# Kernel optimization log

Measured on AMD Instinct MI355X. Metric: run time of the kernel, lower is better.

Reference implementation:

```python
import jax, jax.numpy as jnp
import numpy as np

B, N, H, IN, OUT, AXES = 128, 32, 128, 1, 10, 4


def setup_inputs() -> dict:
    key = jax.random.key(0)
    ks = jax.random.split(key, 6)
    s = 0.05
    return {
        "x": jax.random.normal(ks[0], (B, N, N), jnp.float32),
        "Wx": jax.random.normal(ks[1], (AXES, IN, 3 * H), jnp.float32) * s,
        "U1": jax.random.normal(ks[2], (AXES, H, 3 * H), jnp.float32) * s,
        "U2": jax.random.normal(ks[3], (AXES, H, 3 * H), jnp.float32) * s,
        "b": jnp.zeros((AXES, 3 * H), jnp.float32),
        "Wo": jax.random.normal(ks[4], (AXES * H, OUT), jnp.float32) * s,
        "bo": jnp.zeros((OUT,), jnp.float32),
    }


def _mdgru_cell(xj, h_top, h_left, Wx, U1, U2, b):
    # xj: (B, IN); h_top/h_left: (B, H). Two-predecessor GRU cell.
    gx = xj @ Wx + b          # (B, 3H)
    g1 = h_top @ U1           # (B, 3H)
    g2 = h_left @ U2          # (B, 3H)
    xr, xz, xn = jnp.split(gx, 3, axis=-1)
    r1, z1, n1 = jnp.split(g1, 3, axis=-1)
    r2, z2, n2 = jnp.split(g2, 3, axis=-1)
    r = jax.nn.sigmoid(xr + r1 + r2)
    z = jax.nn.sigmoid(xz + z1 + z2)
    n = jnp.tanh(xn + r * (n1 + n2))
    return (1.0 - z) * n + z * 0.5 * (h_top + h_left)


def _scan_dir(img, Wx, U1, U2, b):
    # img: (N_rows, N_cols, B), oriented so scan runs top-left -> bottom-right.
    n_cols, bsz = img.shape[1], img.shape[2]
    h0 = jnp.zeros((bsz, H), img.dtype)

    def row_step(last_row, x_row):  # last_row: (N_cols, B, H); x_row: (N_cols, B)
        def col_step(h_left, inp):
            xj, h_top = inp
            h = _mdgru_cell(xj[:, None], h_top, h_left, Wx, U1, U2, b)
            return h, h
        _, row = jax.lax.scan(col_step, h0, (x_row, last_row))
        return row, row[-1]

    _, finals = jax.lax.scan(row_step, jnp.zeros((n_cols, bsz, H), img.dtype), img)
    return finals[-1]  # (B, H): hidden at the terminal corner


def reference(x, Wx, U1, U2, b, Wo, bo):
    # x: (B, N, N). Four diagonal scan directions via flips.
    flips = [(False, False), (True, False), (False, True), (True, True)]
    hs = []
    for a, (fi, fj) in enumerate(flips):
        xd = x
        if fi:
            xd = jnp.flip(xd, axis=1)
        if fj:
            xd = jnp.flip(xd, axis=2)
        img = jnp.transpose(xd, (1, 2, 0))  # (N_rows, N_cols, B)
        hs.append(_scan_dir(img, Wx[a], U1[a], U2[a], b[a]))
    final_hidden = jnp.concatenate(hs, axis=1)  # (B, 4H)
    return jax.nn.log_softmax(final_hidden @ Wo + bo, axis=1)
```

## Files before the change

kernel.cpp:

```cpp
#include <hip/hip_runtime.h>
#include <type_traits>


#define B_ 128
#define N_ 32
#define H_ 128
#define TH 384
#define KK 256

#define PLSTR 2640
#define BUFSTR 10560
#define PSTRIDE 21120
#define XDSTR 8064

typedef short bf16x8 __attribute__((ext_vector_type(8)));
typedef float f32x4 __attribute__((ext_vector_type(4)));

__device__ inline ushort f2bf(float f) {
    return (ushort)((__float_as_uint(f) + 0x8000u) >> 16);
}
__device__ inline ushort f2bf_rne(float f) {
    unsigned u = __float_as_uint(f);
    return (ushort)((u + 0x7FFFu + ((u >> 16) & 1u)) >> 16);
}

#define NL2E -1.44269504088896f

__global__ void conv_u(const float* __restrict__ U1, const float* __restrict__ U2,
                       ushort* __restrict__ ubf) {
    __shared__ float t[32][33];
    int bx = blockIdx.x;
    int amat = bx / 48, tile = bx % 48;
    int kt = tile / 12, ntl = tile % 12;
    int a = amat >> 1, mat = amat & 1;
    int kk0 = kt * 32, n0 = ntl * 32;
    int tx = threadIdx.x, ty = threadIdx.y;
    const float* U = mat ? U2 : U1;
#pragma unroll
    for (int r = 0; r < 4; r++)
        t[ty + r * 8][tx] = U[(a * H_ + kk0 + ty + r * 8) * TH + n0 + tx];
    __syncthreads();
#pragma unroll
    for (int r = 0; r < 4; r++) {
        int n = n0 + ty + r * 8;
        int kkl = kk0 + tx;
        ubf[(a * TH + n) * KK + mat * H_ + kkl] = f2bf_rne(t[tx][ty + r * 8]);
    }
}

__global__ __launch_bounds__(512, 2) void scan_all(
    const float* __restrict__ x, const float* __restrict__ Wx,
    const float* __restrict__ bvec, const ushort* __restrict__ ubf,
    float* __restrict__ finals) {

    __shared__ __align__(16) char hbf_c[2 * PSTRIDE];
    __shared__ __align__(16) char xd_c[2 * XDSTR];

    int bx = blockIdx.x;
    int a = bx >> 6, chunk = bx & 63;
    int tid = threadIdx.x;
    int lane = tid & 63, wn = tid >> 6;
    int l16 = lane & 15, lg = lane >> 4;

    for (int idx = tid; idx < (2 * PSTRIDE) / 4; idx += 512) ((unsigned*)hbf_c)[idx] = 0u;
    for (int idx = tid; idx < (2 * XDSTR) / 4; idx += 512) ((unsigned*)xd_c)[idx] = 0u;
    __syncthreads();

    const float* xg = x + (chunk * 2) * (N_ * N_);
    for (int cell = tid; cell < 2048; cell += 512) {
        int P = cell >> 10, c = cell & 1023;
        int i = c >> 5, j = c & 31;
        int ri = (a & 1) ? (31 - i) : i;
        int cj = (a & 2) ? (31 - j) : j;
        *(float*)(xd_c + P * XDSTR + (i + j) * 128 + i * 4) = xg[P * 1024 + ri * 32 + cj];
    }

    const ushort* ub = ubf + a * (TH * KK);
    bf16x8 Bf[3][8];
#pragma unroll
    for (int p = 0; p < 3; p++) {
        int n = p * H_ + wn * 16 + l16;
#pragma unroll
        for (int ks = 0; ks < 8; ks++) {
            Bf[p][ks] = *(const bf16x8*)(ub + n * KK + ks * 32 + lg * 8);
            asm volatile("" : "+v"(Bf[p][ks]));
        }
    }

    int hh = wn * 16 + l16;
    float wxp[3], bsp[3];
    {
        float wr = Wx[a * TH + hh], br = bvec[a * TH + hh];
        float wz = Wx[a * TH + H_ + hh], bz = bvec[a * TH + H_ + hh];
        float wq = Wx[a * TH + 2 * H_ + hh], bq = bvec[a * TH + 2 * H_ + hh];
        wxp[0] = wr * NL2E; bsp[0] = br * NL2E;
        wxp[1] = wz * NL2E; bsp[1] = bz * NL2E;
        wxp[2] = wq;        bsp[2] = bq;
    }

    int aT[2], wbs[2];
#pragma unroll
    for (int mt = 0; mt < 2; mt++) {
        aT[mt] = (mt * 16 + l16) * 80 + lg * 16;
        wbs[mt] = (wn >> 1) * PLSTR + (mt * 16 + lg * 4 + 1) * 80 +
                  ((wn & 1) * 16 + l16) * 2;
    }

    const char* xdp = xd_c + lg * 16;
    __syncthreads();

    float hp[2][2][4];
#pragma unroll
    for (int P = 0; P < 2; P++)
#pragma unroll
        for (int mt = 0; mt < 2; mt++)
#pragma unroll
            for (int r = 0; r < 4; r++) hp[P][mt][r] = 0.0f;

    int slsrc = (lane - 16) & 63;

    auto step = [&](int d, const char* xp, auto WRC) {
        constexpr int WRB = decltype(WRC)::value;
        constexpr int RDB = WRB ^ 1;

        bool gm0 = (d <= 46);
        bool gm1 = (d >= 16);

        f32x4 xv[2][2];
#pragma unroll
        for (int P = 0; P < 2; P++) {
            if (gm0) xv[P][0] = *(const f32x4*)(xp + P * XDSTR);
            if (gm1) xv[P][1] = *(const f32x4*)(xp + P * XDSTR + 64);
        }
        float sh[2][2];
#pragma unroll
        for (int P = 0; P < 2; P++)
#pragma unroll
            for (int mt = 0; mt < 2; mt++)
                sh[P][mt] = __shfl(hp[P][mt][3], slsrc, 64);

        f32x4 acc[2][2][3];
        const f32x4 z4 = {0.0f, 0.0f, 0.0f, 0.0f};

#pragma unroll
        for (int P = 0; P < 2; P++) {
            const char* hbr = hbf_c + P * PSTRIDE + RDB * BUFSTR;
#pragma unroll
            for (int mt = 0; mt < 2; mt++) {
                bool g = mt ? gm1 : gm0;
                if (g) {
                    bf16x8 af[8];
#pragma unroll
                    for (int ks = 0; ks < 4; ks++) {
                        af[ks] = *(const bf16x8*)(hbr + ks * PLSTR + aT[mt]);
                        af[ks + 4] = *(const bf16x8*)(hbr + ks * PLSTR + aT[mt] + 80);
                    }
#pragma unroll
                    for (int ks = 0; ks < 4; ks++)
#pragma unroll
                        for (int p = 0; p < 3; p++)
                            acc[P][mt][p] = __builtin_amdgcn_mfma_f32_16x16x32_bf16(
                                af[ks], Bf[p][ks], (ks == 0) ? z4 : acc[P][mt][p], 0, 0, 0);
#pragma unroll
                    for (int ks = 0; ks < 4; ks++)
#pragma unroll
                        for (int p = 0; p < 3; p++)
                            acc[P][mt][p] = __builtin_amdgcn_mfma_f32_16x16x32_bf16(
                                af[ks + 4], Bf[p][ks + 4], acc[P][mt][p], 0, 0, 0);
                }
            }
        }

#pragma unroll
        for (int P = 0; P < 2; P++) {
            char* hbw = hbf_c + P * PSTRIDE + WRB * BUFSTR;
#pragma unroll
            for (int mt = 0; mt < 2; mt++) {
                bool g = mt ? gm1 : gm0;
                if (g) {
                    float hv[4];
#pragma unroll
                    for (int r = 0; r < 4; r++) {
                        float xb = xv[P][mt][r];
                        float htop = r ? hp[P][mt][r - 1]
                                       : (mt ? (lg ? sh[P][1] : sh[P][0])
                                             : (lg ? sh[P][0] : 0.0f));
                        float hlft = hp[P][mt][r];
                        float Gr = acc[P][mt][0][r];
                        float Gz = acc[P][mt][1][r];
                        float Gn = acc[P][mt][2][r];
                        float ar = __builtin_fmaf(Gr, NL2E, __builtin_fmaf(xb, wxp[0], bsp[0]));
                        float rg = __builtin_amdgcn_rcpf(1.0f + __builtin_amdgcn_exp2f(ar));
                        float az = __builtin_fmaf(Gz, NL2E, __builtin_fmaf(xb, wxp[1], bsp[1]));
                        float ez = __builtin_amdgcn_exp2f(az);
                        float vn = __builtin_fmaf(rg, Gn, __builtin_fmaf(xb, wxp[2], bsp[2]));
                        float en = __builtin_amdgcn_exp2f(vn * (2.0f * NL2E));
                        float pz = 1.0f + ez, pn = 1.0f + en;
                        float rp = __builtin_amdgcn_rcpf(pz * pn);
                        float zg = rp * pn;
                        float ng = __builtin_fmaf(2.0f * rp, pz, -1.0f);
                        float hs = htop + hlft;
                        hv[r] = __builtin_fmaf(-zg, __builtin_fmaf(-0.5f, hs, ng), ng);
                    }
#pragma unroll
                    for (int r = 0; r < 4; r++) {
                        *(ushort*)(hbw + wbs[mt] + r * 80) = f2bf(hv[r]);
                        hp[P][mt][r] = hv[r];
                    }
                }
            }
        }
        __syncthreads();
    };

    const char* xp = xdp;
    for (int d = 0; d < 62; d += 2) {
        step(d, xp, std::integral_constant<int, 0>{});
        step(d + 1, xp + 128, std::integral_constant<int, 1>{});
        xp += 256;
    }
    step(62, xp, std::integral_constant<int, 0>{});

    if (lg == 3) {
        finals[(a * B_ + chunk * 2) * H_ + hh] = hp[0][1][3];
        finals[(a * B_ + chunk * 2 + 1) * H_ + hh] = hp[1][1][3];
    }
}

__global__ void classify(const float* __restrict__ fin, const float* __restrict__ Wo,
                         const float* __restrict__ bo, float* __restrict__ out) {
    int b = blockIdx.x;
    int lane = threadIdx.x;
    float acc[10];
#pragma unroll
    for (int o = 0; o < 10; o++) acc[o] = 0.0f;
#pragma unroll
    for (int kkx = 0; kkx < 8; kkx++) {
        int k = kkx * 64 + lane;
        int a = k >> 7, hh = k & 127;
        float fh = fin[(a * B_ + b) * H_ + hh];
#pragma unroll
        for (int o = 0; o < 10; o++) acc[o] += fh * Wo[k * 10 + o];
    }
    float logits[10];
#pragma unroll
    for (int o = 0; o < 10; o++) {
        float v = acc[o];
#pragma unroll
        for (int off = 32; off; off >>= 1) v += __shfl_xor(v, off, 64);
        logits[o] = v + bo[o];
    }
    float m = logits[0];
#pragma unroll
    for (int o = 1; o < 10; o++) m = fmaxf(m, logits[o]);
    float s = 0.0f;
#pragma unroll
    for (int o = 0; o < 10; o++) s += __expf(logits[o] - m);
    float lse = m + __logf(s);
    if (lane == 0) {
#pragma unroll
        for (int o = 0; o < 10; o++) out[b * 10 + o] = logits[o] - lse;
    }
}

extern "C" void kernel_launch(void* const* d_in, const int* in_sizes, int n_in,
                              void* d_out, int out_size, void* d_ws, size_t ws_size,
                              hipStream_t stream) {
    const float* x = (const float*)d_in[0];
    const float* Wx = (const float*)d_in[1];
    const float* U1 = (const float*)d_in[2];
    const float* U2 = (const float*)d_in[3];
    const float* bv = (const float*)d_in[4];
    const float* Wo = (const float*)d_in[5];
    const float* bo = (const float*)d_in[6];
    float* out = (float*)d_out;

    char* ws = (char*)d_ws;
    ushort* ubf = (ushort*)ws;
    float* finals = (float*)(ws + 786432);

    hipLaunchKernelGGL(conv_u, dim3(384), dim3(32, 8), 0, stream, U1, U2, ubf);
    hipLaunchKernelGGL(scan_all, dim3(256), dim3(512), 0, stream, x, Wx, bv, ubf, finals);
    hipLaunchKernelGGL(classify, dim3(128), dim3(64), 0, stream, finals, Wo, bo, out);
}
```

Before: 173.3 us.

## Switch recurrent GEMM to FP8 MFMA and split blocks to one batch each

Converts the U weights and the hidden-state LDS buffer from bf16 to FP8 (e4m3) and uses the fp8 16x16x32 MFMA. It also drops the two-batches-per-block pairing, so 512 blocks run at one batch each, with launch bounds raised to 4 blocks per CU. The aim is to halve LDS traffic and register footprint and to raise occupancy so more independent scans hide the serial per-diagonal latency. FP8 quantisation of the weights and hidden states adds a lot of numerical error to a 63-step recurrence, which may break accuracy tolerance.

New measurement: 152.3 us. -12.1%, faster.

```diff
diff --git a/kernel.cpp b/kernel.cpp
--- a/kernel.cpp
+++ b/kernel.cpp
@@ -8,26 +8,19 @@
 #define TH 384
 #define KK 256
 
-#define PLSTR 2640
-#define BUFSTR 10560
-#define PSTRIDE 21120
-#define XDSTR 8064
-
-typedef short bf16x8 __attribute__((ext_vector_type(8)));
+#define PLSTR 1320
+#define BUFSTR 5280
+
 typedef float f32x4 __attribute__((ext_vector_type(4)));
 
-__device__ inline ushort f2bf(float f) {
-    return (ushort)((__float_as_uint(f) + 0x8000u) >> 16);
-}
-__device__ inline ushort f2bf_rne(float f) {
-    unsigned u = __float_as_uint(f);
-    return (ushort)((u + 0x7FFFu + ((u >> 16) & 1u)) >> 16);
+__device__ inline unsigned cvt2fp8(float a, float b) {
+    return (unsigned)__builtin_amdgcn_cvt_pk_fp8_f32(a, b, 0, false);
 }
 
 #define NL2E -1.44269504088896f
 
 __global__ void conv_u(const float* __restrict__ U1, const float* __restrict__ U2,
-                       ushort* __restrict__ ubf) {
+                       char* __restrict__ ub8) {
     __shared__ float t[32][33];
     int bx = blockIdx.x;
     int amat = bx / 48, tile = bx % 48;
@@ -44,45 +37,45 @@
     for (int r = 0; r < 4; r++) {
         int n = n0 + ty + r * 8;
         int kkl = kk0 + tx;
-        ubf[(a * TH + n) * KK + mat * H_ + kkl] = f2bf_rne(t[tx][ty + r * 8]);
-    }
-}
-
-__global__ __launch_bounds__(512, 2) void scan_all(
+        unsigned pk = cvt2fp8(t[tx][ty + r * 8], 0.0f);
+        ub8[(a * TH + n) * KK + mat * H_ + kkl] = (char)(pk & 0xFF);
+    }
+}
+
+__global__ __launch_bounds__(512, 4) void scan_all(
     const float* __restrict__ x, const float* __restrict__ Wx,
-    const float* __restrict__ bvec, const ushort* __restrict__ ubf,
+    const float* __restrict__ bvec, const char* __restrict__ ubf8,
     float* __restrict__ finals) {
 
-    __shared__ __align__(16) char hbf_c[2 * PSTRIDE];
-    __shared__ __align__(16) char xd_c[2 * XDSTR];
+    __shared__ __align__(16) char hbf_c[2 * BUFSTR];
+    __shared__ __align__(16) float xd[63 * 32];
 
     int bx = blockIdx.x;
-    int a = bx >> 6, chunk = bx & 63;
+    int a = bx >> 7, b = bx & 127;
     int tid = threadIdx.x;
     int lane = tid & 63, wn = tid >> 6;
     int l16 = lane & 15, lg = lane >> 4;
 
-    for (int idx = tid; idx < (2 * PSTRIDE) / 4; idx += 512) ((unsigned*)hbf_c)[idx] = 0u;
-    for (int idx = tid; idx < (2 * XDSTR) / 4; idx += 512) ((unsigned*)xd_c)[idx] = 0u;
+    for (int idx = tid; idx < (2 * BUFSTR) / 4; idx += 512) ((unsigned*)hbf_c)[idx] = 0u;
+    for (int idx = tid; idx < 63 * 32; idx += 512) xd[idx] = 0.0f;
     __syncthreads();
 
-    const float* xg = x + (chunk * 2) * (N_ * N_);
-    for (int cell = tid; cell < 2048; cell += 512) {
-        int P = cell >> 10, c = cell & 1023;
-        int i = c >> 5, j = c & 31;
+    const float* xg = x + b * (N_ * N_);
+    for (int cell = tid; cell < 1024; cell += 512) {
+        int i = cell >> 5, j = cell & 31;
         int ri = (a & 1) ? (31 - i) : i;
         int cj = (a & 2) ? (31 - j) : j;
-        *(float*)(xd_c + P * XDSTR + (i + j) * 128 + i * 4) = xg[P * 1024 + ri * 32 + cj];
-    }
-
-    const ushort* ub = ubf + a * (TH * KK);
-    bf16x8 Bf[3][8];
+        xd[(i + j) * 32 + i] = xg[ri * 32 + cj];
+    }
+
+    const char* ub = ubf8 + a * (TH * KK);
+    long Bf[3][8];
 #pragma unroll
     for (int p = 0; p < 3; p++) {
         int n = p * H_ + wn * 16 + l16;
 #pragma unroll
         for (int ks = 0; ks < 8; ks++) {
-            Bf[p][ks] = *(const bf16x8*)(ub + n * KK + ks * 32 + lg * 8);
+            Bf[p][ks] = *(const long*)(ub + n * KK + ks * 32 + lg * 8);
             asm volatile("" : "+v"(Bf[p][ks]));
         }
     }
@@ -101,113 +94,102 @@
     int aT[2], wbs[2];
 #pragma unroll
     for (int mt = 0; mt < 2; mt++) {
-        aT[mt] = (mt * 16 + l16) * 80 + lg * 16;
-        wbs[mt] = (wn >> 1) * PLSTR + (mt * 16 + lg * 4 + 1) * 80 +
-                  ((wn & 1) * 16 + l16) * 2;
-    }
-
-    const char* xdp = xd_c + lg * 16;
+        aT[mt] = (mt * 16 + l16) * 40 + lg * 8;
+        wbs[mt] = (wn >> 1) * PLSTR + (mt * 16 + lg * 4 + 1) * 40 + (wn & 1) * 16 + l16;
+    }
+
+    const char* xdp = (const char*)xd + lg * 16;
     __syncthreads();
 
-    float hp[2][2][4];
-#pragma unroll
-    for (int P = 0; P < 2; P++)
-#pragma unroll
-        for (int mt = 0; mt < 2; mt++)
-#pragma unroll
-            for (int r = 0; r < 4; r++) hp[P][mt][r] = 0.0f;
+    float hp[2][4];
+#pragma unroll
+    for (int mt = 0; mt < 2; mt++)
+#pragma unroll
+        for (int r = 0; r < 4; r++) hp[mt][r] = 0.0f;
 
     int slsrc = (lane - 16) & 63;
 
     auto step = [&](int d, const char* xp, auto WRC) {
         constexpr int WRB = decltype(WRC)::value;
         constexpr int RDB = WRB ^ 1;
+        const char* hbr = hbf_c + RDB * BUFSTR;
+        char* hbw = hbf_c + WRB * BUFSTR;
 
         bool gm0 = (d <= 46);
         bool gm1 = (d >= 16);
 
-        f32x4 xv[2][2];
-#pragma unroll
-        for (int P = 0; P < 2; P++) {
-            if (gm0) xv[P][0] = *(const f32x4*)(xp + P * XDSTR);
-            if (gm1) xv[P][1] = *(const f32x4*)(xp + P * XDSTR + 64);
-        }
-        float sh[2][2];
-#pragma unroll
-        for (int P = 0; P < 2; P++)
-#pragma unroll
-            for (int mt = 0; mt < 2; mt++)
-                sh[P][mt] = __shfl(hp[P][mt][3], slsrc, 64);
-
-        f32x4 acc[2][2][3];
+        f32x4 xv[2];
+        if (gm0) xv[0] = *(const f32x4*)(xp);
+        if (gm1) xv[1] = *(const f32x4*)(xp + 64);
+        float sh[2];
+#pragma unroll
+        for (int mt = 0; mt < 2; mt++) sh[mt] = __shfl(hp[mt][3], slsrc, 64);
+
+        f32x4 acc[2][3];
         const f32x4 z4 = {0.0f, 0.0f, 0.0f, 0.0f};
 
 #pragma unroll
-        for (int P = 0; P < 2; P++) {
-            const char* hbr = hbf_c + P * PSTRIDE + RDB * BUFSTR;
-#pragma unroll
-            for (int mt = 0; mt < 2; mt++) {
-                bool g = mt ? gm1 : gm0;
-                if (g) {
-                    bf16x8 af[8];
-#pragma unroll
-                    for (int ks = 0; ks < 4; ks++) {
-                        af[ks] = *(const bf16x8*)(hbr + ks * PLSTR + aT[mt]);
-                        af[ks + 4] = *(const bf16x8*)(hbr + ks * PLSTR + aT[mt] + 80);
-                    }
-#pragma unroll
-                    for (int ks = 0; ks < 4; ks++)
-#pragma unroll
-                        for (int p = 0; p < 3; p++)
-                            acc[P][mt][p] = __builtin_amdgcn_mfma_f32_16x16x32_bf16(
-                                af[ks], Bf[p][ks], (ks == 0) ? z4 : acc[P][mt][p], 0, 0, 0);
-#pragma unroll
-                    for (int ks = 0; ks < 4; ks++)
-#pragma unroll
-                        for (int p = 0; p < 3; p++)
-                            acc[P][mt][p] = __builtin_amdgcn_mfma_f32_16x16x32_bf16(
-                                af[ks + 4], Bf[p][ks + 4], acc[P][mt][p], 0, 0, 0);
+        for (int mt = 0; mt < 2; mt++) {
+            bool g = mt ? gm1 : gm0;
+            if (g) {
+                long af[8];
+#pragma unroll
+                for (int ks = 0; ks < 4; ks++) {
+                    af[ks] = *(const long*)(hbr + ks * PLSTR + aT[mt]);
+                    af[ks + 4] = *(const long*)(hbr + ks * PLSTR + aT[mt] + 40);
                 }
+#pragma unroll
+                for (int ks = 0; ks < 4; ks++)
+#pragma unroll
+                    for (int p = 0; p < 3; p++)
+                        acc[mt][p] = __builtin_amdgcn_mfma_f32_16x16x32_fp8_fp8(
+                            af[ks], Bf[p][ks], (ks == 0) ? z4 : acc[mt][p], 0, 0, 0);
+#pragma unroll
+                for (int ks = 0; ks < 4; ks++)
+#pragma unroll
+                    for (int p = 0; p < 3; p++)
+                        acc[mt][p] = __builtin_amdgcn_mfma_f32_16x16x32_fp8_fp8(
+                            af[ks + 4], Bf[p][ks + 4], acc[mt][p], 0, 0, 0);
             }
         }
 
 #pragma unroll
-        for (int P = 0; P < 2; P++) {
-            char* hbw = hbf_c + P * PSTRIDE + WRB * BUFSTR;
-#pragma unroll
-            for (int mt = 0; mt < 2; mt++) {
-                bool g = mt ? gm1 : gm0;
-                if (g) {
-                    float hv[4];
-#pragma unroll
-                    for (int r = 0; r < 4; r++) {
-                        float xb = xv[P][mt][r];
-                        float htop = r ? hp[P][mt][r - 1]
-                                       : (mt ? (lg ? sh[P][1] : sh[P][0])
-                                             : (lg ? sh[P][0] : 0.0f));
-                        float hlft = hp[P][mt][r];
-                        float Gr = acc[P][mt][0][r];
-                        float Gz = acc[P][mt][1][r];
-                        float Gn = acc[P][mt][2][r];
-                        float ar = __builtin_fmaf(Gr, NL2E, __builtin_fmaf(xb, wxp[0], bsp[0]));
-                        float rg = __builtin_amdgcn_rcpf(1.0f + __builtin_amdgcn_exp2f(ar));
-                        float az = __builtin_fmaf(Gz, NL2E, __builtin_fmaf(xb, wxp[1], bsp[1]));
-                        float ez = __builtin_amdgcn_exp2f(az);
-                        float vn = __builtin_fmaf(rg, Gn, __builtin_fmaf(xb, wxp[2], bsp[2]));
-                        float en = __builtin_amdgcn_exp2f(vn * (2.0f * NL2E));
-                        float pz = 1.0f + ez, pn = 1.0f + en;
-                        float rp = __builtin_amdgcn_rcpf(pz * pn);
-                        float zg = rp * pn;
-                        float ng = __builtin_fmaf(2.0f * rp, pz, -1.0f);
-                        float hs = htop + hlft;
-                        hv[r] = __builtin_fmaf(-zg, __builtin_fmaf(-0.5f, hs, ng), ng);
-                    }
-#pragma unroll
-                    for (int r = 0; r < 4; r++) {
-                        *(ushort*)(hbw + wbs[mt] + r * 80) = f2bf(hv[r]);
-                        hp[P][mt][r] = hv[r];
-                    }
+        for (int mt = 0; mt < 2; mt++) {
+            bool g = mt ? gm1 : gm0;
+            if (g) {
+                float hv[4];
+#pragma unroll
+                for (int r = 0; r < 4; r++) {
+                    float xb = xv[mt][r];
+                    float htop = r ? hp[mt][r - 1]
+                                   : (mt ? (lg ? sh[1] : sh[0])
+                                         : (lg ? sh[0] : 0.0f));
+                    float hlft = hp[mt][r];
+                    float Gr = acc[mt][0][r];
+                    float Gz = acc[mt][1][r];
+                    float Gn = acc[mt][2][r];
+                    float ar = __builtin_fmaf(Gr, NL2E, __builtin_fmaf(xb, wxp[0], bsp[0]));
+                    float rg = __builtin_amdgcn_rcpf(1.0f + __builtin_amdgcn_exp2f(ar));
+                    float az = __builtin_fmaf(Gz, NL2E, __builtin_fmaf(xb, wxp[1], bsp[1]));
+                    float ez = __builtin_amdgcn_exp2f(az);
+                    float vn = __builtin_fmaf(rg, Gn, __builtin_fmaf(xb, wxp[2], bsp[2]));
+                    float en = __builtin_amdgcn_exp2f(vn * (2.0f * NL2E));
+                    float pz = 1.0f + ez, pn = 1.0f + en;
+                    float rp = __builtin_amdgcn_rcpf(pz * pn);
+                    float zg = rp * pn;
+                    float ng = __builtin_fmaf(2.0f * rp, pz, -1.0f);
+                    float hs = htop + hlft;
+                    hv[r] = __builtin_fmaf(-zg, __builtin_fmaf(-0.5f, hs, ng), ng);
                 }
+                unsigned pk01 = cvt2fp8(hv[0], hv[1]);
+                unsigned pk23 = cvt2fp8(hv[2], hv[3]);
+                char* wp = hbw + wbs[mt];
+                wp[0] = (char)(pk01 & 0xFF);
+                wp[40] = (char)((pk01 >> 8) & 0xFF);
+                wp[80] = (char)(pk23 & 0xFF);
+                wp[120] = (char)((pk23 >> 8) & 0xFF);
+#pragma unroll
+                for (int r = 0; r < 4; r++) hp[mt][r] = hv[r];
             }
         }
         __syncthreads();
@@ -221,10 +203,7 @@
     }
     step(62, xp, std::integral_constant<int, 0>{});
 
-    if (lg == 3) {
-        finals[(a * B_ + chunk * 2) * H_ + hh] = hp[0][1][3];
-        finals[(a * B_ + chunk * 2 + 1) * H_ + hh] = hp[1][1][3];
-    }
+    if (lg == 3) finals[(a * B_ + b) * H_ + hh] = hp[1][3];
 }
 
 __global__ void classify(const float* __restrict__ fin, const float* __restrict__ Wo,
@@ -276,10 +255,10 @@
     float* out = (float*)d_out;
 
     char* ws = (char*)d_ws;
-    ushort* ubf = (ushort*)ws;
-    float* finals = (float*)(ws + 786432);
-
-    hipLaunchKernelGGL(conv_u, dim3(384), dim3(32, 8), 0, stream, U1, U2, ubf);
-    hipLaunchKernelGGL(scan_all, dim3(256), dim3(512), 0, stream, x, Wx, bv, ubf, finals);
+    char* ub8 = ws;
+    float* finals = (float*)(ws + 393216);
+
+    hipLaunchKernelGGL(conv_u, dim3(384), dim3(32, 8), 0, stream, U1, U2, ub8);
+    hipLaunchKernelGGL(scan_all, dim3(512), dim3(512), 0, stream, x, Wx, bv, ub8, finals);
     hipLaunchKernelGGL(classify, dim3(128), dim3(64), 0, stream, finals, Wo, bo, out);
 }
```
